# Kernel optimization log

Measured on AMD Instinct MI355X. Metric: run time of the kernel, lower is better.

## Reference

```python
import jax, jax.numpy as jnp
import numpy as np

TAU = 2.0      # LIF time constant
VTH = 1.0      # spike threshold
ALPHA = 4.0    # sigmoid surrogate slope (spikingjelly default)
EPS = 1e-5     # BN eps

@jax.custom_vjp
def spike_fn(x):
    return (x >= 0.0).astype(x.dtype)

def _spike_fwd(x):
    return spike_fn(x), x

def _spike_bwd(x, g):
    s = jax.nn.sigmoid(ALPHA * x)
    return (g * ALPHA * s * (1.0 - s),)

spike_fn.defvjp(_spike_fwd, _spike_bwd)

def conv2d(x, w, stride=1):
    return jax.lax.conv_general_dilated(
        x, w, (stride, stride), 'SAME',
        dimension_numbers=('NCHW', 'OIHW', 'NCHW'))

def bn(x, g, b, m, v):
    # eval-mode BatchNorm2d over channel axis 1
    scale = g / jnp.sqrt(v + EPS)
    return (x - m[:, None, None]) * scale[:, None, None] + b[:, None, None]

def lif_step(v, x):
    # charge, fire, hard reset to 0 (detach_reset)
    v = v + (x - v) / TAU
    s = spike_fn(v - VTH)
    v = (1.0 - jax.lax.stop_gradient(s)) * v
    return v, s

def lif_multistep(x_seq):
    v0 = jnp.zeros_like(x_seq[0])
    _, s = jax.lax.scan(lif_step, v0, x_seq)
    return s

def setup_inputs():
    key = jax.random.key(0)
    ks = jax.random.split(key, 8)
    T, B, C, H, W = 4, 4, 2, 128, 128
    E = 256
    x = jax.random.normal(ks[0], (T, B, C, H, W), jnp.float32)
    w_proj = jax.random.normal(ks[1], (E // 2, C, 3, 3), jnp.float32) * 0.2
    w_temp = jax.random.normal(ks[2], (C, E // 2, 3, 3), jnp.float32) * 0.05
    w1 = jax.random.normal(ks[3], (E, E // 2, 3, 3), jnp.float32) * 0.03
    w_res = jax.random.normal(ks[4], (E, E // 2, 1, 1), jnp.float32) * 0.09
    def bn_params(k, c):
        kk = jax.random.split(k, 2)
        return (jnp.abs(jax.random.normal(kk[0], (c,), jnp.float32)) + 0.5,
                jax.random.normal(kk[1], (c,), jnp.float32) * 0.1,
                jnp.zeros((c,), jnp.float32), jnp.ones((c,), jnp.float32))
    g0, b0, m0, v0 = bn_params(ks[5], E // 2)
    gt, bt, mt, vt = bn_params(ks[6], C)
    g1, b1, m1, v1 = bn_params(ks[7], E)
    gr, br, mr, vr = bn_params(jax.random.fold_in(key, 99), E)
    return dict(x=x, w_proj=w_proj, g0=g0, b0=b0, m0=m0, v0=v0,
                w_temp=w_temp, gt=gt, bt=bt, mt=mt, vt=vt,
                w1=w1, g1=g1, b1=b1, m1=m1, v1=v1,
                w_res=w_res, gr=gr, br=br, mr=mr, vr=vr)

def reference(x, w_proj, g0, b0, m0, v0, w_temp, gt, bt, mt, vt,
              w1, g1, b1, m1, v1, w_res, gr, br, mr, vr):
    T, B, C, H, W = x.shape
    half = w_proj.shape[0]
    # stf_1 recurrent coding: x_in[t] = x[t] + x_out[t-1]; LIF states persist
    def step(carry, x_t):
        x_out, vp, vtm = carry
        x_in = x_t + x_out
        h = bn(conv2d(x_in, w_proj), g0, b0, m0, v0)          # [B,half,H,W]
        vp, s1 = lif_step(vp, h)                              # proj_lif
        y = bn(conv2d(s1, w_temp), gt, bt, mt, vt)            # [B,C,H,W]
        vtm, s2 = lif_step(vtm, y)                            # proj_temporal_lif
        return (s2, vp, vtm), s1
    init = (jnp.zeros((B, C, H, W), x.dtype),
            jnp.zeros((B, half, H, W), x.dtype),
            jnp.zeros((B, C, H, W), x.dtype))
    _, spikes = jax.lax.scan(step, init, x)                   # [T,B,half,H,W]
    xf = spikes.reshape(T * B, half, H, W)
    xa = bn(conv2d(xf, w1), g1, b1, m1, v1).reshape(T, B, -1, H, W)
    xa = lif_multistep(xa)                                    # proj1_lif
    xr = bn(conv2d(xf, w_res), gr, br, mr, vr).reshape(T, B, -1, H, W)
    xr = lif_multistep(xr)                                    # proj_res_lif
    return xa + xr
```

## Files before the change

kernel.cpp:

```cpp
#include <hip/hip_runtime.h>
#include <math.h>

#define HW 16384

typedef __attribute__((ext_vector_type(8))) _Float16 half8;
typedef __attribute__((ext_vector_type(4))) float f32x4;

__global__ __launch_bounds__(256)
void k_reorder2(const float* __restrict__ w1, const float* __restrict__ wres,
                const float* __restrict__ g1, const float* __restrict__ b1,
                const float* __restrict__ m1, const float* __restrict__ v1,
                const float* __restrict__ gr, const float* __restrict__ br,
                const float* __restrict__ mr, const float* __restrict__ vr,
                short* __restrict__ whi, short* __restrict__ wmid,
                short* __restrict__ rhi, short* __restrict__ rmid,
                float* __restrict__ bias1, float* __restrict__ biasr) {
    int i = blockIdx.x * 256 + threadIdx.x;
    if (i < 294912) {
        int n = i / 1152, rem = i % 1152;
        int ic = rem / 9, tap = rem % 9;
        float sc = g1[n] / sqrtf(v1[n] + 1e-5f);
        float wv = (w1[i] * sc) * 4096.0f;
        _Float16 h = (_Float16)wv;
        float r1 = wv - (float)h;
        _Float16 m = (_Float16)r1;
        int kb = ic >> 5, q = (ic >> 3) & 3, j = ic & 7;
        size_t f = ((((size_t)(kb * 9 + tap)) * 4 + q) * 256 + n) * 8 + j;
        whi[f]  = __builtin_bit_cast(short, h);
        wmid[f] = __builtin_bit_cast(short, m);
    }
    if (i < 32768) {
        int n = i >> 7, ic = i & 127;
        float sc = gr[n] / sqrtf(vr[n] + 1e-5f);
        float wv = (wres[i] * sc) * 4096.0f;
        _Float16 h = (_Float16)wv;
        float r1 = wv - (float)h;
        _Float16 m = (_Float16)r1;
        int kb = ic >> 5, q = (ic >> 3) & 3, j = ic & 7;
        size_t f = (((size_t)kb * 4 + q) * 256 + n) * 8 + j;
        rhi[f]  = __builtin_bit_cast(short, h);
        rmid[f] = __builtin_bit_cast(short, m);
    }
    if (i < 256) {
        float sc1 = g1[i] / sqrtf(v1[i] + 1e-5f);
        bias1[i] = (b1[i] - m1[i] * sc1) * 4096.0f;
        float scr_ = gr[i] / sqrtf(vr[i] + 1e-5f);
        biasr[i] = (br[i] - mr[i] * scr_) * 4096.0f;
    }
}

__global__ __launch_bounds__(256)
void k_proj(const float* __restrict__ xt, const float* __restrict__ xout,
            const float* __restrict__ wp,
            const float* __restrict__ g, const float* __restrict__ bb,
            const float* __restrict__ mm, const float* __restrict__ vv,
            float* __restrict__ vp, unsigned char* __restrict__ s1t, int first) {
    __shared__ float xin[2 * 10 * 36];
    const int tid = threadIdx.x;
    const int b   = blockIdx.z >> 2;
    const int ocq = blockIdx.z & 3;
    const int gy0 = blockIdx.y * 8, gx0 = blockIdx.x * 32;

    for (int i = tid; i < 680; i += 256) {
        int ch = i / 340, rem = i % 340;
        int r = rem / 34, c = rem % 34;
        int gy = gy0 - 1 + r, gx = gx0 - 1 + c;
        float val = 0.f;
        if (gy >= 0 && gy < 128 && gx >= 0 && gx < 128) {
            int idx = ((b * 2 + ch) << 14) + (gy << 7) + gx;
            val = xt[idx];
            if (!first) val += xout[idx];
        }
        xin[(ch * 10 + r) * 36 + c] = val;
    }
    __syncthreads();

    const int prow = tid >> 5, pcol = tid & 31;
    float xw[2][3][3];
#pragma unroll
    for (int ch = 0; ch < 2; ++ch)
#pragma unroll
        for (int ky = 0; ky < 3; ++ky)
#pragma unroll
            for (int kx = 0; kx < 3; ++kx)
                xw[ch][ky][kx] = xin[(ch * 10 + prow + ky) * 36 + pcol + kx];

    const int pix = ((gy0 + prow) << 7) + gx0 + pcol;
    const int oc_beg = ocq * 32;
    unsigned int pk = 0u;
#pragma unroll
    for (int oo = 0; oo < 32; ++oo) {
        const int oc = oc_beg + oo;
        float acc = 0.f;
#pragma unroll
        for (int ch = 0; ch < 2; ++ch)
#pragma unroll
            for (int ky = 0; ky < 3; ++ky)
#pragma unroll
                for (int kx = 0; kx < 3; ++kx)
                    acc = fmaf(wp[((oc * 2 + ch) * 3 + ky) * 3 + kx], xw[ch][ky][kx], acc);
        float sc = g[oc] / sqrtf(vv[oc] + 1e-5f);
        float h  = (acc - mm[oc]) * sc + bb[oc];
        int idx = ((b * 128 + oc) << 14) + pix;
        float v = first ? 0.f : vp[idx];
        v = v + (h - v) * 0.5f;
        bool s = (v >= 1.0f);
        vp[idx] = s ? 0.f : v;
        pk |= (s ? 1u : 0u) << oo;
    }
    *(unsigned int*)(s1t + ((((size_t)b << 14) + pix) << 4) + ocq * 4) = pk;
}

__global__ __launch_bounds__(256)
void k_temp(const unsigned char* __restrict__ s1t, const float* __restrict__ wt,
            const float* __restrict__ g, const float* __restrict__ bb,
            const float* __restrict__ mm, const float* __restrict__ vv,
            float* __restrict__ vtm, float* __restrict__ xout, int first) {
    __shared__ unsigned char sl[49152];
    __shared__ float wls[2304];
    __shared__ float red[256];
    const int tid = threadIdx.x;
    const int b   = blockIdx.y;
    const int y0  = blockIdx.x;

    for (int i = tid; i < 2304; i += 256) wls[i] = wt[i];

    for (int i = tid; i < 384; i += 256) {
        int r = i >> 7, px = i & 127;
        int gy = y0 - 1 + r;
        uint4 d = make_uint4(0u, 0u, 0u, 0u);
        if (gy >= 0 && gy < 128)
            d = *(const uint4*)(s1t + ((((size_t)b << 14) + (gy << 7) + px) << 4));
        unsigned int bs[4] = {d.x, d.y, d.z, d.w};
#pragma unroll
        for (int icb = 0; icb < 16; ++icb) {
            unsigned int v8 = (bs[icb >> 2] >> ((icb & 3) * 8)) & 0xFFu;
            unsigned int lo = (v8 & 1u) | ((v8 & 2u) << 7) | ((v8 & 4u) << 14) | ((v8 & 8u) << 21);
            unsigned int hi = ((v8 >> 4) & 1u) | ((v8 & 32u) << 3) | ((v8 & 64u) << 10) | ((v8 & 128u) << 17);
            *(uint2*)&sl[(((icb * 3) + r) * 128 + (px ^ (icb & 7))) * 8] = make_uint2(lo, hi);
        }
    }
    __syncthreads();

    const int x = tid & 127, hf = tid >> 7;
    float a0 = 0.f, a1 = 0.f;
#pragma unroll 1
    for (int ii = 0; ii < 8; ++ii) {
        const int icb = hf * 8 + ii;
        int sw = icb & 7;
        const float* w0 = &wls[icb * 72];
        const float* w1_ = &wls[1152 + icb * 72];
#pragma unroll
        for (int dy = 0; dy < 3; ++dy) {
#pragma unroll
            for (int dx = 0; dx < 3; ++dx) {
                int xx = x - 1 + dx;
                if (xx < 0 || xx > 127) continue;
                uint2 d = *(const uint2*)&sl[((icb * 3 + dy) * 128 + (xx ^ sw)) * 8];
                int tap = dy * 3 + dx;
#pragma unroll
                for (int j = 0; j < 4; ++j) {
                    float f0 = (float)((d.x >> (8 * j)) & 0xFFu);
                    float f1 = (float)((d.y >> (8 * j)) & 0xFFu);
                    a0 = fmaf(w0[j * 9 + tap],        f0, a0);
                    a0 = fmaf(w0[(4 + j) * 9 + tap],  f1, a0);
                    a1 = fmaf(w1_[j * 9 + tap],       f0, a1);
                    a1 = fmaf(w1_[(4 + j) * 9 + tap], f1, a1);
                }
            }
        }
    }
    if (hf) { red[x] = a0; red[128 + x] = a1; }
    __syncthreads();
    if (!hf) {
        a0 += red[x]; a1 += red[128 + x];
#pragma unroll
        for (int oc = 0; oc < 2; ++oc) {
            float acc = (oc == 0) ? a0 : a1;
            float sc = g[oc] / sqrtf(vv[oc] + 1e-5f);
            float yv = (acc - mm[oc]) * sc + bb[oc];
            int idx = ((b * 2 + oc) << 14) + (y0 << 7) + x;
            float v = first ? 0.f : vtm[idx];
            v = v + (yv - v) * 0.5f;
            bool s = (v >= 1.0f);
            vtm[idx]  = s ? 0.f : v;
            xout[idx] = s ? 1.0f : 0.f;
        }
    }
}

__global__ __launch_bounds__(256, 3)
void k_fused(const unsigned char* __restrict__ s1c,
             const short* __restrict__ whi, const short* __restrict__ wmid,
             const short* __restrict__ rhi, const short* __restrict__ rmid,
             const float* __restrict__ bias1, const float* __restrict__ biasr,
             float* __restrict__ out) {
    __shared__ __align__(16) unsigned char bl[8704];

    const int tid = threadIdx.x;
    const int oc0 = blockIdx.x * 64;
    const int yb = blockIdx.y;
    const int b = yb >> 8, ry = (yb >> 2) & 63, cx = yb & 3;
    const int gy0 = ry * 2, gx0 = cx * 32;

    const int w   = tid >> 6, l = tid & 63;
    const int q   = l >> 4,  ln = l & 15;
    const int woc = w >> 1,  wpx = w & 1;

    const size_t wofs = ((size_t)q * 256 + oc0 + woc * 32 + ln) * 8;

    int pb[2], po[2];
#pragma unroll
    for (int nt = 0; nt < 2; ++nt) {
        int px = wpx * 32 + nt * 16 + ln;
        int prow = px >> 5, pcol = px & 31;
        pb[nt] = prow * 34 + pcol;
        po[nt] = ((gy0 + prow) << 7) + gx0 + pcol;
    }

    for (int cc = tid; cc < 544; cc += 256) {
        int t = cc / 136, p = cc - t * 136;
        int r = p / 34, c = p - r * 34;
        int gy = gy0 - 1 + r, gx = gx0 - 1 + c;
        uint4 d = make_uint4(0u, 0u, 0u, 0u);
        if (gy >= 0 && gy < 128 && gx >= 0 && gx < 128)
            d = *(const uint4*)(s1c + (size_t)t * 1048576 +
                                ((((size_t)b << 14) + (gy << 7) + gx) << 4));
        *(uint4*)(bl + cc * 16) = d;
    }
    __syncthreads();

    const float ds_ = 0.000244140625f;

    unsigned int srb[4];
    {
        f32x4 brr[2];
#pragma unroll
        for (int mt = 0; mt < 2; ++mt)
#pragma unroll
            for (int rg = 0; rg < 4; ++rg)
                brr[mt][rg] = biasr[oc0 + woc * 32 + mt * 16 + q * 4 + rg];

        float vres[2][2][4];
#pragma unroll
        for (int nt = 0; nt < 2; ++nt)
#pragma unroll
            for (int mt = 0; mt < 2; ++mt)
#pragma unroll
                for (int rg = 0; rg < 4; ++rg) vres[nt][mt][rg] = 0.f;

#pragma unroll
        for (int t = 0; t < 4; ++t) {
            const unsigned char* blt = bl + t * 2176;
            f32x4 accr[2][2];
#pragma unroll
            for (int nt = 0; nt < 2; ++nt)
#pragma unroll
                for (int mt = 0; mt < 2; ++mt) accr[nt][mt] = brr[mt];

#pragma unroll
            for (int kb = 0; kb < 4; ++kb) {
                half8 B4[2];
#pragma unroll
                for (int nt = 0; nt < 2; ++nt) {
                    unsigned int v8 = blt[(pb[nt] + 35) * 16 + kb * 4 + q];
                    uint4 pk;
                    pk.x = ((v8 & 1u)          | ((v8 & 2u)   << 15)) * 0x3C00u;
                    pk.y = (((v8 >> 2) & 1u)   | ((v8 & 8u)   << 13)) * 0x3C00u;
                    pk.z = (((v8 >> 4) & 1u)   | ((v8 & 32u)  << 11)) * 0x3C00u;
                    pk.w = (((v8 >> 6) & 1u)   | ((v8 & 128u) << 9 )) * 0x3C00u;
                    B4[nt] = __builtin_bit_cast(half8, pk);
                }
                half8 RH[2], RM[2];
#pragma unroll
                for (int mt = 0; mt < 2; ++mt) {
                    RH[mt] = *(const half8*)(rhi  + wofs + (size_t)kb * 8192 + mt * 128);
                    RM[mt] = *(const half8*)(rmid + wofs + (size_t)kb * 8192 + mt * 128);
                }
#pragma unroll
                for (int nt = 0; nt < 2; ++nt)
#pragma unroll
                    for (int mt = 0; mt < 2; ++mt) {
                        accr[nt][mt] = __builtin_amdgcn_mfma_f32_16x16x32_f16(RH[mt], B4[nt], accr[nt][mt], 0, 0, 0);
                        accr[nt][mt] = __builtin_amdgcn_mfma_f32_16x16x32_f16(RM[mt], B4[nt], accr[nt][mt], 0, 0, 0);
                    }
            }

            unsigned int sb = 0u;
#pragma unroll
            for (int nt = 0; nt < 2; ++nt)
#pragma unroll
                for (int mt = 0; mt < 2; ++mt)
#pragma unroll
                    for (int rg = 0; rg < 4; ++rg) {
                        float hr = accr[nt][mt][rg] * ds_;
                        float u = vres[nt][mt][rg];
                        u = u + (hr - u) * 0.5f;
                        bool sr_ = (u >= 1.0f);
                        vres[nt][mt][rg] = sr_ ? 0.f : u;
                        sb |= (sr_ ? 1u : 0u) << (mt * 8 + rg * 2 + nt);
                    }
            srb[t] = sb;
        }
    }

    f32x4 acc[4][2][2];
#pragma unroll
    for (int mt = 0; mt < 2; ++mt)
#pragma unroll
        for (int rg = 0; rg < 4; ++rg) {
            float bv = bias1[oc0 + woc * 32 + mt * 16 + q * 4 + rg];
#pragma unroll
            for (int t = 0; t < 4; ++t)
#pragma unroll
                for (int nt = 0; nt < 2; ++nt) acc[t][nt][mt][rg] = bv;
        }

    const short* bh = whi  + wofs;
    const short* bm = wmid + wofs;
#pragma unroll 1
    for (int kb = 0; kb < 4; ++kb) {
        const int byi = kb * 4 + q;
#pragma unroll
        for (int tap = 0; tap < 9; ++tap) {
            const int ky = tap / 3, kx = tap % 3;
            half8 AH[2], AM[2];
#pragma unroll
            for (int mt = 0; mt < 2; ++mt) {
                AH[mt] = *(const half8*)(bh + mt * 128);
                AM[mt] = *(const half8*)(bm + mt * 128);
            }
#pragma unroll
            for (int t = 0; t < 4; ++t) {
                const unsigned char* blt = bl + t * 2176;
                half8 B4[2];
#pragma unroll
                for (int nt = 0; nt < 2; ++nt) {
                    unsigned int v8 = blt[(pb[nt] + ky * 34 + kx) * 16 + byi];
                    uint4 pk;
                    pk.x = ((v8 & 1u)          | ((v8 & 2u)   << 15)) * 0x3C00u;
                    pk.y = (((v8 >> 2) & 1u)   | ((v8 & 8u)   << 13)) * 0x3C00u;
                    pk.z = (((v8 >> 4) & 1u)   | ((v8 & 32u)  << 11)) * 0x3C00u;
                    pk.w = (((v8 >> 6) & 1u)   | ((v8 & 128u) << 9 )) * 0x3C00u;
                    B4[nt] = __builtin_bit_cast(half8, pk);
                }
#pragma unroll
                for (int nt = 0; nt < 2; ++nt)
#pragma unroll
                    for (int mt = 0; mt < 2; ++mt) {
                        acc[t][nt][mt] = __builtin_amdgcn_mfma_f32_16x16x32_f16(AH[mt], B4[nt], acc[t][nt][mt], 0, 0, 0);
                        acc[t][nt][mt] = __builtin_amdgcn_mfma_f32_16x16x32_f16(AM[mt], B4[nt], acc[t][nt][mt], 0, 0, 0);
                    }
            }
            bh += 8192; bm += 8192;
        }
    }

    float va[2][2][4];
#pragma unroll
    for (int nt = 0; nt < 2; ++nt)
#pragma unroll
        for (int mt = 0; mt < 2; ++mt)
#pragma unroll
            for (int rg = 0; rg < 4; ++rg) va[nt][mt][rg] = 0.f;

#pragma unroll
    for (int t = 0; t < 4; ++t) {
        const size_t tb = ((size_t)((t * 4 + b) * 256 + oc0)) << 14;
#pragma unroll
        for (int mt = 0; mt < 2; ++mt)
#pragma unroll
            for (int rg = 0; rg < 4; ++rg) {
                const size_t ob = tb + ((size_t)(woc * 32 + mt * 16 + q * 4 + rg) << 14);
#pragma unroll
                for (int nt = 0; nt < 2; ++nt) {
                    float ha = acc[t][nt][mt][rg] * ds_;
                    float v = va[nt][mt][rg];
                    v = v + (ha - v) * 0.5f;
                    bool s = (v >= 1.0f);
                    va[nt][mt][rg] = s ? 0.f : v;
                    float sa = s ? 1.f : 0.f;
                    float sr = ((srb[t] >> (mt * 8 + rg * 2 + nt)) & 1u) ? 1.f : 0.f;
                    out[ob + po[nt]] = sa + sr;
                }
            }
    }
}

extern "C" void kernel_launch(void* const* d_in, const int* in_sizes, int n_in,
                              void* d_out, int out_size, void* d_ws, size_t ws_size,
                              hipStream_t stream) {
    const float* x      = (const float*)d_in[0];
    const float* w_proj = (const float*)d_in[1];
    const float* g0 = (const float*)d_in[2];
    const float* b0 = (const float*)d_in[3];
    const float* m0 = (const float*)d_in[4];
    const float* v0 = (const float*)d_in[5];
    const float* w_temp = (const float*)d_in[6];
    const float* gt = (const float*)d_in[7];
    const float* bt = (const float*)d_in[8];
    const float* mt = (const float*)d_in[9];
    const float* vt = (const float*)d_in[10];
    const float* w1 = (const float*)d_in[11];
    const float* g1 = (const float*)d_in[12];
    const float* b1 = (const float*)d_in[13];
    const float* m1 = (const float*)d_in[14];
    const float* v1 = (const float*)d_in[15];
    const float* w_res = (const float*)d_in[16];
    const float* gr = (const float*)d_in[17];
    const float* br = (const float*)d_in[18];
    const float* mr = (const float*)d_in[19];
    const float* vr = (const float*)d_in[20];

    char* ws = (char*)d_ws;
    unsigned char* s1c = (unsigned char*)ws;
    float* vp    = (float*)(ws + 4194304);
    float* vtm   = (float*)(ws + 37748736);
    float* xout  = (float*)(ws + 38273024);
    short* whi   = (short*)(ws + 38797312);
    short* wmid  = (short*)(ws + 39387136);
    short* rhi   = (short*)(ws + 39976960);
    short* rmid  = (short*)(ws + 40042496);
    float* bias1 = (float*)(ws + 40108032);
    float* biasr = (float*)(ws + 40109056);

    k_reorder2<<<dim3(1152), dim3(256), 0, stream>>>(
        w1, w_res, g1, b1, m1, v1, gr, br, mr, vr,
        whi, wmid, rhi, rmid, bias1, biasr);

    for (int t = 0; t < 4; ++t) {
        const float* xt = x + (size_t)t * 131072;
        unsigned char* s1t = s1c + (size_t)t * 1048576;
        k_proj<<<dim3(4, 16, 16), dim3(256), 0, stream>>>(
            xt, xout, w_proj, g0, b0, m0, v0, vp, s1t, t == 0);
        k_temp<<<dim3(128, 4), dim3(256), 0, stream>>>(
            s1t, w_temp, gt, bt, mt, vt, vtm, xout, t == 0);
    }

    k_fused<<<dim3(4, 1024), dim3(256), 0, stream>>>(
        s1c, whi, wmid, rhi, rmid, bias1, biasr, (float*)d_out);
}
```

Measured before the change: 689.8 us.

## Pre-expand bit-packed spikes to fp16 in shared memory per K-block

Each K-block now starts by decoding the bit-packed spike bytes into fp16 half8 vectors in a new 43.5 KB shared buffer, with barriers around the expansion. The MFMA loop then reads B operands as plain 16-byte LDS loads instead of redoing the byte load and bit-unpack for every tap and timestep. This removes repeated VALU decode work (nine taps reuse each decoded pixel) at the cost of much more LDS per block, likely lowering occupancy below the launch-bounds target of three blocks, and adding extra syncs per K-block.

```diff
diff --git a/kernel.cpp b/kernel.cpp
--- a/kernel.cpp
+++ b/kernel.cpp
@@ -196,6 +196,7 @@
              const float* __restrict__ bias1, const float* __restrict__ biasr,
              float* __restrict__ out) {
     __shared__ __align__(16) unsigned char bl[8704];
+    __shared__ __align__(16) unsigned char xp[43520];
 
     const int tid = threadIdx.x;
     const int oc0 = blockIdx.x * 64;
@@ -209,13 +210,14 @@
 
     const size_t wofs = ((size_t)q * 256 + oc0 + woc * 32 + ln) * 8;
 
-    int pb[2], po[2];
+    int pb[2], po[2], eb[2];
 #pragma unroll
     for (int nt = 0; nt < 2; ++nt) {
         int px = wpx * 32 + nt * 16 + ln;
         int prow = px >> 5, pcol = px & 31;
         pb[nt] = prow * 34 + pcol;
         po[nt] = ((gy0 + prow) << 7) + gx0 + pcol;
+        eb[nt] = pb[nt] * 80 + q * 16;
     }
 
     for (int cc = tid; cc < 544; cc += 256) {
@@ -320,10 +322,27 @@
     const short* bm = wmid + wofs;
 #pragma unroll 1
     for (int kb = 0; kb < 4; ++kb) {
-        const int byi = kb * 4 + q;
+        if (kb) __syncthreads();
+        for (int cc = tid; cc < 544; cc += 256) {
+            unsigned int wd = *(const unsigned int*)(bl + cc * 16 + kb * 4);
+            int t = cc / 136, p = cc - t * 136;
+            unsigned char* dst = xp + t * 10880 + p * 80;
+#pragma unroll
+            for (int c2 = 0; c2 < 4; ++c2) {
+                unsigned int x0 = wd >> (8 * c2);
+                uint4 o;
+                o.x = ((x0 & 1u)          | ((x0 & 2u)   << 15)) * 0x3C00u;
+                o.y = (((x0 >> 2) & 1u)   | ((x0 & 8u)   << 13)) * 0x3C00u;
+                o.z = (((x0 >> 4) & 1u)   | ((x0 & 32u)  << 11)) * 0x3C00u;
+                o.w = (((x0 >> 6) & 1u)   | ((x0 & 128u) << 9 )) * 0x3C00u;
+                *(uint4*)(dst + c2 * 16) = o;
+            }
+        }
+        __syncthreads();
+
 #pragma unroll
         for (int tap = 0; tap < 9; ++tap) {
-            const int ky = tap / 3, kx = tap % 3;
+            const int toff = ((tap / 3) * 34 + (tap % 3)) * 80;
             half8 AH[2], AM[2];
 #pragma unroll
             for (int mt = 0; mt < 2; ++mt) {
@@ -332,18 +351,10 @@
             }
 #pragma unroll
             for (int t = 0; t < 4; ++t) {
-                const unsigned char* blt = bl + t * 2176;
                 half8 B4[2];
 #pragma unroll
-                for (int nt = 0; nt < 2; ++nt) {
-                    unsigned int v8 = blt[(pb[nt] + ky * 34 + kx) * 16 + byi];
-                    uint4 pk;
-                    pk.x = ((v8 & 1u)          | ((v8 & 2u)   << 15)) * 0x3C00u;
-                    pk.y = (((v8 >> 2) & 1u)   | ((v8 & 8u)   << 13)) * 0x3C00u;
-                    pk.z = (((v8 >> 4) & 1u)   | ((v8 & 32u)  << 11)) * 0x3C00u;
-                    pk.w = (((v8 >> 6) & 1u)   | ((v8 & 128u) << 9 )) * 0x3C00u;
-                    B4[nt] = __builtin_bit_cast(half8, pk);
-                }
+                for (int nt = 0; nt < 2; ++nt)
+                    B4[nt] = *(const half8*)(xp + t * 10880 + eb[nt] + toff);
 #pragma unroll
                 for (int nt = 0; nt < 2; ++nt)
 #pragma unroll
```

Result: faster. 630.3 us (-8.6%).
